# Kernel optimization log

Measured on AMD Instinct MI355X. Metric: run time of the kernel, lower is better.

The kernel has to match this reference:

```python
import jax, jax.numpy as jnp
import numpy as np
from functools import partial

D, H, W = 32, 256, 256   # grid_size (D, H, W)
V = 40000                # number of active voxels
C_IN, C_OUT = 16, 32
K = 3                    # kernel size
P = 32                   # max_points per voxel
EPS = 1e-5               # BatchNorm eps


def setup_inputs() -> dict:
    key = jax.random.key(0)
    k1, k2, k3, k4 = jax.random.split(key, 4)
    voxels = jax.random.normal(k1, (V, C_IN, P), dtype=jnp.float32)
    lin = jax.random.choice(k2, D * H * W, (V,), replace=False)
    d = (lin // (H * W)).astype(jnp.int32)
    h = ((lin // W) % H).astype(jnp.int32)
    w = (lin % W).astype(jnp.int32)
    indices = jnp.stack([w, h, d], axis=1)  # columns are (w, h, d) per original usage
    conv_w = jax.random.normal(k3, (C_OUT, C_IN, K, K, K), dtype=jnp.float32) * 0.05
    conv_b = jax.random.normal(k4, (C_OUT,), dtype=jnp.float32) * 0.05
    gamma = jnp.ones((C_OUT,), dtype=jnp.float32)
    beta = jnp.zeros((C_OUT,), dtype=jnp.float32)
    return {"voxels": voxels, "indices": indices, "conv_w": conv_w,
            "conv_b": conv_b, "gamma": gamma, "beta": beta, "batch_size": 1}


def reference(voxels, indices, conv_w, conv_b, gamma, beta, batch_size):
    # voxel features: mean over points  [V, C]
    feats = voxels.mean(axis=2)
    w_i, h_i, d_i = indices[:, 0], indices[:, 1], indices[:, 2]
    # original: batch_mask = indices[:,0] >= 0, plus per-dim bounds check
    valid = ((w_i >= 0) & (w_i < W) & (h_i >= 0) & (h_i < H) & (d_i >= 0) & (d_i < D))
    d_s = jnp.where(valid, d_i, D)  # route invalid rows out-of-bounds -> dropped
    # fused scatter replacing the python per-voxel loop; [D, H, W, C]
    grid = jnp.zeros((D, H, W, C_IN), dtype=voxels.dtype).at[d_s, h_i, w_i].set(
        feats, mode="drop")
    # same scatter is written into every batch slice in the original
    dense = jnp.broadcast_to(jnp.transpose(grid, (3, 0, 1, 2))[None],
                             (batch_size, C_IN, D, H, W))
    # Conv3d, padding = K//2 (SAME)
    out = jax.lax.conv_general_dilated(
        dense, conv_w, window_strides=(1, 1, 1), padding=[(K // 2, K // 2)] * 3,
        dimension_numbers=("NCDHW", "OIDHW", "NCDHW"))
    out = out + conv_b[None, :, None, None, None]
    # BatchNorm3d (training-mode batch statistics, biased variance)
    mean = out.mean(axis=(0, 2, 3, 4), keepdims=True)
    var = out.var(axis=(0, 2, 3, 4), keepdims=True)
    out = (out - mean) * jax.lax.rsqrt(var + EPS)
    out = out * gamma[None, :, None, None, None] + beta[None, :, None, None, None]
    return jax.nn.relu(out)
```

## Files before the change

### kernel.cpp

```cpp
#include <hip/hip_runtime.h>

#define D_   32
#define H_   256
#define W_   256
#define HW_  (H_ * W_)
#define DHW_ (D_ * H_ * W_)
#define V_   40000
#define CIN  16
#define COUT 32
#define P_   32
#define EPS_ 1e-5f

#define TD 2
#define TH 8
#define TW 32
#define NTX (W_ / TW)
#define NTY (H_ / TH)
#define NTZ (D_ / TD)
#define NT  (NTX * NTY * NTZ)
#define TPOS (TD * TH * TW)
#define OH 16
#define TAP_CAP 768

__global__ void bin_count_kernel(const int* __restrict__ idxs, int* __restrict__ counts) {
    int v = blockIdx.x * 256 + threadIdx.x;
    if (v >= V_) return;
    int w = idxs[3 * v], h = idxs[3 * v + 1], d = idxs[3 * v + 2];
    if ((unsigned)w < W_ && (unsigned)h < H_ && (unsigned)d < D_) {
        int b = (d / TD) * NTY * NTX + (h / TH) * NTX + (w / TW);
        atomicAdd(&counts[b], 1);
    }
}

__global__ void scan_kernel(const int* __restrict__ counts, int* __restrict__ starts,
                            int* __restrict__ cursor, const float* __restrict__ conv_w,
                            float4* __restrict__ wt4) {
    __shared__ int part[256];
    int t = threadIdx.x;
    int base = t * 16;
    int s = 0;
    for (int j = 0; j < 16; ++j) s += counts[base + j];
    part[t] = s;
    __syncthreads();
    for (int off = 1; off < 256; off <<= 1) {
        int val = part[t];
        int add = (t >= off) ? part[t - off] : 0;
        __syncthreads();
        part[t] = val + add;
        __syncthreads();
    }
    int run = (t > 0) ? part[t - 1] : 0;
    for (int j = 0; j < 16; ++j) {
        starts[base + j] = run;
        cursor[base + j] = run;
        run += counts[base + j];
    }
    for (int n = t; n < 2 * 27 * 4 * 16; n += 256) {
        int oo = n & 15;
        int jj = (n >> 4) & 3;
        int m  = n >> 6;
        int k  = m % 27;
        int half = m / 27;
        int o = half * 16 + oo;
        float4 wv;
        wv.x = conv_w[(o * CIN + 4 * jj + 0) * 27 + k];
        wv.y = conv_w[(o * CIN + 4 * jj + 1) * 27 + k];
        wv.z = conv_w[(o * CIN + 4 * jj + 2) * 27 + k];
        wv.w = conv_w[(o * CIN + 4 * jj + 3) * 27 + k];
        wt4[n] = wv;
    }
}

__global__ void bin_fill_kernel(const int* __restrict__ idxs, int* __restrict__ cursor,
                                int* __restrict__ pos_packed, int* __restrict__ perm) {
    int v = blockIdx.x * 256 + threadIdx.x;
    if (v >= V_) return;
    int w = idxs[3 * v], h = idxs[3 * v + 1], d = idxs[3 * v + 2];
    if ((unsigned)w < W_ && (unsigned)h < H_ && (unsigned)d < D_) {
        int b = (d / TD) * NTY * NTX + (h / TH) * NTX + (w / TW);
        int p = atomicAdd(&cursor[b], 1);
        pos_packed[p] = (d << 16) | (h << 8) | w;
        perm[v] = p;
    }
}

__global__ void featpack_kernel(const float* __restrict__ vox, const int* __restrict__ idxs,
                                const int* __restrict__ perm, float4* __restrict__ feats4) {
    int idx = blockIdx.x * 256 + threadIdx.x;
    if (idx >= V_ * 4) return;
    int v = idx >> 2, q = idx & 3;
    int w = idxs[3 * v], h = idxs[3 * v + 1], d = idxs[3 * v + 2];
    if (!((unsigned)w < W_ && (unsigned)h < H_ && (unsigned)d < D_)) return;
    int slot = perm[v];
    const float* base = vox + ((size_t)v * CIN + 4 * q) * P_;
    float m[4];
#pragma unroll
    for (int c = 0; c < 4; ++c) {
        const float4* p = (const float4*)(base + c * P_);
        float s = 0.f;
#pragma unroll
        for (int j = 0; j < P_ / 4; ++j) {
            float4 t = p[j];
            s += t.x + t.y + t.z + t.w;
        }
        m[c] = s * (1.0f / (float)P_);
    }
    feats4[slot * 4 + q] = make_float4(m[0], m[1], m[2], m[3]);
}

__global__ void __launch_bounds__(256, 2) tile_conv_kernel(
    const float4* __restrict__ feats4, const float4* __restrict__ wt4,
    const int* __restrict__ starts, const int* __restrict__ counts,
    const int* __restrict__ pos_packed, float* __restrict__ stats,
    float* __restrict__ out)
{
    __shared__ float  tile[TPOS * 16];
    __shared__ float4 wsm4[27 * 4 * 16];
    __shared__ int    taps[TAP_CAP];
    __shared__ int    seg_off[28];
    __shared__ int    seg_gs[27];
    __shared__ float  wsum[4][16], wsq[4][16];
    __shared__ int    ntap;

    int t = threadIdx.x;
    int tile_id = blockIdx.x;
    int half = blockIdx.y;
    int tx = tile_id % NTX, ty = (tile_id / NTX) % NTY, tz = tile_id / (NTX * NTY);
    int w0 = tx * TW, h0 = ty * TH, d0 = tz * TD;
    int obase = half * OH;

    for (int j = t; j < TPOS * 16 / 4; j += 256) ((float4*)tile)[j] = make_float4(0, 0, 0, 0);
    for (int j = t; j < 27 * 4 * 16; j += 256) wsm4[j] = wt4[half * (27 * 4 * 16) + j];
    if (t < 27) {
        int dz = t / 9 - 1, dy = (t / 3) % 3 - 1, dx = t % 3 - 1;
        int nz = tz + dz, ny = ty + dy, nx = tx + dx;
        int cnt = 0, gs = 0;
        if ((unsigned)nz < NTZ && (unsigned)ny < NTY && (unsigned)nx < NTX) {
            int b = nz * NTY * NTX + ny * NTX + nx;
            gs = starts[b];
            cnt = counts[b];
        }
        seg_gs[t] = gs;
        seg_off[t] = cnt;
    }
    if (t == 0) ntap = 0;
    __syncthreads();
    if (t == 0) {
        int run = 0;
#pragma unroll
        for (int i = 0; i < 27; ++i) {
            int c = seg_off[i];
            seg_off[i] = run;
            run += c;
        }
        seg_off[27] = run;
    }
    __syncthreads();
    int ncand = seg_off[27];

    for (int j = t; j < ncand; j += 256) {
        int b = 0;
        while (seg_off[b + 1] <= j) ++b;
        int src = seg_gs[b] + (j - seg_off[b]);
        int pp = pos_packed[src];
        int vw = pp & 255, vh = (pp >> 8) & 255, vd = pp >> 16;
        int dlo = max(vd - 1, d0), dhi = min(vd + 1, d0 + TD - 1);
        int hlo = max(vh - 1, h0), hhi = min(vh + 1, h0 + TH - 1);
        int wlo = max(vw - 1, w0), whi = min(vw + 1, w0 + TW - 1);
        for (int dq = dlo; dq <= dhi; ++dq)
            for (int hq = hlo; hq <= hhi; ++hq)
                for (int wq = wlo; wq <= whi; ++wq) {
                    int k = ((vd - dq + 1) * 3 + (vh - hq + 1)) * 3 + (vw - wq + 1);
                    int pos = ((dq - d0) * TH + (hq - h0)) * TW + (wq - w0);
                    int slot2 = atomicAdd(&ntap, 1);
                    if (slot2 < TAP_CAP) taps[slot2] = (src << 14) | (k << 9) | pos;
                }
    }
    __syncthreads();
    int nt = min(ntap, TAP_CAP);

    int oo = t & 15;
    int slot = t >> 4;
    for (int j = slot; j < nt; j += 16) {
        unsigned tap = (unsigned)taps[j];
        int pos = tap & 511;
        int k = (tap >> 9) & 31;
        int src = tap >> 14;
        const float4* fp = feats4 + src * 4;
        float4 f0 = fp[0], f1 = fp[1], f2 = fp[2], f3 = fp[3];
        const float4* wp = &wsm4[(k * 4) * 16 + oo];
        float4 q0 = wp[0], q1 = wp[16], q2 = wp[32], q3 = wp[48];
        float acc = q0.x * f0.x + q0.y * f0.y + q0.z * f0.z + q0.w * f0.w
                  + q1.x * f1.x + q1.y * f1.y + q1.z * f1.z + q1.w * f1.w
                  + q2.x * f2.x + q2.y * f2.y + q2.z * f2.z + q2.w * f2.w
                  + q3.x * f3.x + q3.y * f3.y + q3.z * f3.z + q3.w * f3.w;
        atomicAdd(&tile[pos * 16 + (oo ^ (pos & 15))], acc);
    }
    __syncthreads();

    float s1 = 0.f, s2 = 0.f;
    for (int p = slot; p < TPOS; p += 16) {
        float sv = tile[p * 16 + (oo ^ (p & 15))];
        s1 += sv;
        s2 += sv * sv;
    }
    s1 += __shfl_xor(s1, 16); s2 += __shfl_xor(s2, 16);
    s1 += __shfl_xor(s1, 32); s2 += __shfl_xor(s2, 32);
    int wave = t >> 6, lane = t & 63;
    if (lane < 16) { wsum[wave][lane] = s1; wsq[wave][lane] = s2; }

    int wl = t & 31;
    for (int r = t >> 5; r < OH * TD * TH; r += 8) {
        int oo2 = r >> 4;
        int rem = r & 15;
        int pos = rem * TW + wl;
        int dl = rem >> 3, hl = rem & 7;
        out[(size_t)(obase + oo2) * DHW_ + (size_t)(d0 + dl) * HW_ +
            (size_t)(h0 + hl) * W_ + (w0 + wl)] = tile[pos * 16 + (oo2 ^ (pos & 15))];
    }
    __syncthreads();
    if (t < 16) {
        float a = wsum[0][t] + wsum[1][t] + wsum[2][t] + wsum[3][t];
        float b = wsq[0][t] + wsq[1][t] + wsq[2][t] + wsq[3][t];
        atomicAdd(&stats[obase + t], a);
        atomicAdd(&stats[COUT + obase + t], b);
    }
}

__global__ void finalize_kernel(const float* __restrict__ stats,
                                const float* __restrict__ gamma,
                                const float* __restrict__ beta,
                                float* __restrict__ mi) {
    int t = threadIdx.x;
    if (t < COUT) {
        float n = (float)DHW_;
        float m1 = stats[t] / n;
        float m2 = stats[COUT + t] / n;
        float var = fmaxf(m2 - m1 * m1, 0.f);
        float inv = rsqrtf(var + EPS_);
        float A = gamma[t] * inv;
        mi[t] = A;
        mi[COUT + t] = -m1 * A + beta[t];
    }
}

__global__ void norm_kernel(float* __restrict__ out, const float* __restrict__ mi) {
    int idx4 = blockIdx.x * 256 + threadIdx.x;
    int c = idx4 >> 19;
    float A = mi[c], B = mi[COUT + c];
    float4 x = ((const float4*)out)[idx4];
    x.x = fmaxf(x.x * A + B, 0.f);
    x.y = fmaxf(x.y * A + B, 0.f);
    x.z = fmaxf(x.z * A + B, 0.f);
    x.w = fmaxf(x.w * A + B, 0.f);
    ((float4*)out)[idx4] = x;
}

extern "C" void kernel_launch(void* const* d_in, const int* in_sizes, int n_in,
                              void* d_out, int out_size, void* d_ws, size_t ws_size,
                              hipStream_t stream) {
    const float* voxels  = (const float*)d_in[0];
    const int*   indices = (const int*)  d_in[1];
    const float* conv_w  = (const float*)d_in[2];
    const float* gamma   = (const float*)d_in[4];
    const float* beta    = (const float*)d_in[5];
    float* out = (float*)d_out;

    float4* wt4     = (float4*)d_ws;
    float4* feats4  = wt4 + 3456;
    int*    counts  = (int*)(feats4 + (size_t)V_ * 4);
    int*    starts  = counts + NT;
    int*    cursor  = starts + NT;
    int*    pos_pk  = cursor + NT;
    int*    perm    = pos_pk + V_;
    float*  stats   = (float*)(perm + V_);
    float*  mi      = stats + 2 * COUT;

    hipMemsetAsync(counts, 0, NT * sizeof(int), stream);
    hipMemsetAsync(stats, 0, 2 * COUT * sizeof(float), stream);

    bin_count_kernel<<<(V_ + 255) / 256, 256, 0, stream>>>(indices, counts);
    scan_kernel<<<1, 256, 0, stream>>>(counts, starts, cursor, conv_w, wt4);
    bin_fill_kernel<<<(V_ + 255) / 256, 256, 0, stream>>>(indices, cursor, pos_pk, perm);
    featpack_kernel<<<(V_ * 4 + 255) / 256, 256, 0, stream>>>(voxels, indices, perm, feats4);

    dim3 grid(NT, 2);
    tile_conv_kernel<<<grid, 256, 0, stream>>>(feats4, wt4, starts, counts, pos_pk,
                                               stats, out);
    finalize_kernel<<<1, 64, 0, stream>>>(stats, gamma, beta, mi);

    const int n4 = COUT * DHW_ / 4;
    norm_kernel<<<n4 / 256, 256, 0, stream>>>(out, mi);
}
```

Baseline: 752.2 us.

## Precompute global tap lists and recompute conv to fuse BN+ReLU into output write

Replaces per-tile candidate gathering with a global scatter of taps into per-tile lists, built from a count/scan/fill pass over voxels. The conv kernel now runs twice: the first pass only gathers BN statistics without writing output, and the second recomputes the sparse conv and writes the normalized, ReLU'd result directly. This removes the separate norm kernel's full read-modify-write over the large dense output. Feature means are now computed in voxel order, so the permutation step goes away. The cost is recomputing the sparse conv and a larger global tap buffer, and blocks move to 512 threads.

```diff
diff --git a/kernel.cpp b/kernel.cpp
--- a/kernel.cpp
+++ b/kernel.cpp
@@ -20,15 +20,37 @@
 #define NT  (NTX * NTY * NTZ)
 #define TPOS (TD * TH * TW)
 #define OH 16
-#define TAP_CAP 768
-
-__global__ void bin_count_kernel(const int* __restrict__ idxs, int* __restrict__ counts) {
+
+__global__ void feats_kernel(const float* __restrict__ vox, float* __restrict__ feats) {
+    int idx = blockIdx.x * 256 + threadIdx.x;
+    if (idx >= V_ * CIN) return;
+    const float4* p = (const float4*)(vox + (size_t)idx * P_);
+    float s = 0.f;
+#pragma unroll
+    for (int j = 0; j < P_ / 4; ++j) {
+        float4 q = p[j];
+        s += q.x + q.y + q.z + q.w;
+    }
+    feats[idx] = s * (1.0f / (float)P_);
+}
+
+__global__ void tap_count_kernel(const int* __restrict__ idxs, int* __restrict__ counts) {
     int v = blockIdx.x * 256 + threadIdx.x;
     if (v >= V_) return;
     int w = idxs[3 * v], h = idxs[3 * v + 1], d = idxs[3 * v + 2];
-    if ((unsigned)w < W_ && (unsigned)h < H_ && (unsigned)d < D_) {
-        int b = (d / TD) * NTY * NTX + (h / TH) * NTX + (w / TW);
-        atomicAdd(&counts[b], 1);
+    if (!((unsigned)w < W_ && (unsigned)h < H_ && (unsigned)d < D_)) return;
+    int dlo = max(d - 1, 0), dhi = min(d + 1, D_ - 1);
+    int hlo = max(h - 1, 0), hhi = min(h + 1, H_ - 1);
+    int wlo = max(w - 1, 0), whi = min(w + 1, W_ - 1);
+    for (int tz = dlo / TD; tz <= dhi / TD; ++tz) {
+        int nd = min(dhi, tz * TD + TD - 1) - max(dlo, tz * TD) + 1;
+        for (int ty = hlo / TH; ty <= hhi / TH; ++ty) {
+            int nh = min(hhi, ty * TH + TH - 1) - max(hlo, ty * TH) + 1;
+            for (int tx = wlo / TW; tx <= whi / TW; ++tx) {
+                int nw = min(whi, tx * TW + TW - 1) - max(wlo, tx * TW) + 1;
+                atomicAdd(&counts[(tz * NTY + ty) * NTX + tx], nd * nh * nw);
+            }
+        }
     }
 }
 
@@ -71,56 +93,46 @@
     }
 }
 
-__global__ void bin_fill_kernel(const int* __restrict__ idxs, int* __restrict__ cursor,
-                                int* __restrict__ pos_packed, int* __restrict__ perm) {
+__global__ void tap_fill_kernel(const int* __restrict__ idxs, int* __restrict__ cursor,
+                                int* __restrict__ taps_g) {
     int v = blockIdx.x * 256 + threadIdx.x;
     if (v >= V_) return;
     int w = idxs[3 * v], h = idxs[3 * v + 1], d = idxs[3 * v + 2];
-    if ((unsigned)w < W_ && (unsigned)h < H_ && (unsigned)d < D_) {
-        int b = (d / TD) * NTY * NTX + (h / TH) * NTX + (w / TW);
-        int p = atomicAdd(&cursor[b], 1);
-        pos_packed[p] = (d << 16) | (h << 8) | w;
-        perm[v] = p;
-    }
-}
-
-__global__ void featpack_kernel(const float* __restrict__ vox, const int* __restrict__ idxs,
-                                const int* __restrict__ perm, float4* __restrict__ feats4) {
-    int idx = blockIdx.x * 256 + threadIdx.x;
-    if (idx >= V_ * 4) return;
-    int v = idx >> 2, q = idx & 3;
-    int w = idxs[3 * v], h = idxs[3 * v + 1], d = idxs[3 * v + 2];
     if (!((unsigned)w < W_ && (unsigned)h < H_ && (unsigned)d < D_)) return;
-    int slot = perm[v];
-    const float* base = vox + ((size_t)v * CIN + 4 * q) * P_;
-    float m[4];
-#pragma unroll
-    for (int c = 0; c < 4; ++c) {
-        const float4* p = (const float4*)(base + c * P_);
-        float s = 0.f;
-#pragma unroll
-        for (int j = 0; j < P_ / 4; ++j) {
-            float4 t = p[j];
-            s += t.x + t.y + t.z + t.w;
-        }
-        m[c] = s * (1.0f / (float)P_);
-    }
-    feats4[slot * 4 + q] = make_float4(m[0], m[1], m[2], m[3]);
-}
-
-__global__ void __launch_bounds__(256, 2) tile_conv_kernel(
+    int dlo = max(d - 1, 0), dhi = min(d + 1, D_ - 1);
+    int hlo = max(h - 1, 0), hhi = min(h + 1, H_ - 1);
+    int wlo = max(w - 1, 0), whi = min(w + 1, W_ - 1);
+    for (int tz = dlo / TD; tz <= dhi / TD; ++tz) {
+        int sdlo = max(dlo, tz * TD), sdhi = min(dhi, tz * TD + TD - 1);
+        for (int ty = hlo / TH; ty <= hhi / TH; ++ty) {
+            int shlo = max(hlo, ty * TH), shhi = min(hhi, ty * TH + TH - 1);
+            for (int tx = wlo / TW; tx <= whi / TW; ++tx) {
+                int swlo = max(wlo, tx * TW), swhi = min(whi, tx * TW + TW - 1);
+                int cnt = (sdhi - sdlo + 1) * (shhi - shlo + 1) * (swhi - swlo + 1);
+                int p = atomicAdd(&cursor[(tz * NTY + ty) * NTX + tx], cnt);
+                for (int dq = sdlo; dq <= sdhi; ++dq)
+                    for (int hq = shlo; hq <= shhi; ++hq)
+                        for (int wq = swlo; wq <= swhi; ++wq) {
+                            int k = ((d - dq + 1) * 3 + (h - hq + 1)) * 3 + (w - wq + 1);
+                            int pos = ((dq - tz * TD) * TH + (hq - ty * TH)) * TW +
+                                      (wq - tx * TW);
+                            taps_g[p++] = (v << 14) | (k << 9) | pos;
+                        }
+            }
+        }
+    }
+}
+
+template <int PASS>
+__global__ void __launch_bounds__(512, 4) tile_conv_kernel(
     const float4* __restrict__ feats4, const float4* __restrict__ wt4,
     const int* __restrict__ starts, const int* __restrict__ counts,
-    const int* __restrict__ pos_packed, float* __restrict__ stats,
-    float* __restrict__ out)
+    const int* __restrict__ taps_g, float* __restrict__ stats,
+    const float* __restrict__ mi, float* __restrict__ out)
 {
     __shared__ float  tile[TPOS * 16];
     __shared__ float4 wsm4[27 * 4 * 16];
-    __shared__ int    taps[TAP_CAP];
-    __shared__ int    seg_off[28];
-    __shared__ int    seg_gs[27];
-    __shared__ float  wsum[4][16], wsq[4][16];
-    __shared__ int    ntap;
+    __shared__ float  wsum[8][16], wsq[8][16];
 
     int t = threadIdx.x;
     int tile_id = blockIdx.x;
@@ -129,60 +141,17 @@
     int w0 = tx * TW, h0 = ty * TH, d0 = tz * TD;
     int obase = half * OH;
 
-    for (int j = t; j < TPOS * 16 / 4; j += 256) ((float4*)tile)[j] = make_float4(0, 0, 0, 0);
-    for (int j = t; j < 27 * 4 * 16; j += 256) wsm4[j] = wt4[half * (27 * 4 * 16) + j];
-    if (t < 27) {
-        int dz = t / 9 - 1, dy = (t / 3) % 3 - 1, dx = t % 3 - 1;
-        int nz = tz + dz, ny = ty + dy, nx = tx + dx;
-        int cnt = 0, gs = 0;
-        if ((unsigned)nz < NTZ && (unsigned)ny < NTY && (unsigned)nx < NTX) {
-            int b = nz * NTY * NTX + ny * NTX + nx;
-            gs = starts[b];
-            cnt = counts[b];
-        }
-        seg_gs[t] = gs;
-        seg_off[t] = cnt;
-    }
-    if (t == 0) ntap = 0;
+    for (int j = t; j < TPOS * 16 / 4; j += 512) ((float4*)tile)[j] = make_float4(0, 0, 0, 0);
+    for (int j = t; j < 27 * 4 * 16; j += 512) wsm4[j] = wt4[half * (27 * 4 * 16) + j];
     __syncthreads();
-    if (t == 0) {
-        int run = 0;
-#pragma unroll
-        for (int i = 0; i < 27; ++i) {
-            int c = seg_off[i];
-            seg_off[i] = run;
-            run += c;
-        }
-        seg_off[27] = run;
-    }
-    __syncthreads();
-    int ncand = seg_off[27];
-
-    for (int j = t; j < ncand; j += 256) {
-        int b = 0;
-        while (seg_off[b + 1] <= j) ++b;
-        int src = seg_gs[b] + (j - seg_off[b]);
-        int pp = pos_packed[src];
-        int vw = pp & 255, vh = (pp >> 8) & 255, vd = pp >> 16;
-        int dlo = max(vd - 1, d0), dhi = min(vd + 1, d0 + TD - 1);
-        int hlo = max(vh - 1, h0), hhi = min(vh + 1, h0 + TH - 1);
-        int wlo = max(vw - 1, w0), whi = min(vw + 1, w0 + TW - 1);
-        for (int dq = dlo; dq <= dhi; ++dq)
-            for (int hq = hlo; hq <= hhi; ++hq)
-                for (int wq = wlo; wq <= whi; ++wq) {
-                    int k = ((vd - dq + 1) * 3 + (vh - hq + 1)) * 3 + (vw - wq + 1);
-                    int pos = ((dq - d0) * TH + (hq - h0)) * TW + (wq - w0);
-                    int slot2 = atomicAdd(&ntap, 1);
-                    if (slot2 < TAP_CAP) taps[slot2] = (src << 14) | (k << 9) | pos;
-                }
-    }
-    __syncthreads();
-    int nt = min(ntap, TAP_CAP);
-
-    int oo = t & 15;
+
+    int base = starts[tile_id];
+    int cnt  = counts[tile_id];
+    int oo   = t & 15;
     int slot = t >> 4;
-    for (int j = slot; j < nt; j += 16) {
-        unsigned tap = (unsigned)taps[j];
+
+    for (int j = slot; j < cnt; j += 32) {
+        unsigned tap = (unsigned)taps_g[base + j];
         int pos = tap & 511;
         int k = (tap >> 9) & 31;
         int src = tap >> 14;
@@ -198,32 +167,38 @@
     }
     __syncthreads();
 
-    float s1 = 0.f, s2 = 0.f;
-    for (int p = slot; p < TPOS; p += 16) {
-        float sv = tile[p * 16 + (oo ^ (p & 15))];
-        s1 += sv;
-        s2 += sv * sv;
-    }
-    s1 += __shfl_xor(s1, 16); s2 += __shfl_xor(s2, 16);
-    s1 += __shfl_xor(s1, 32); s2 += __shfl_xor(s2, 32);
-    int wave = t >> 6, lane = t & 63;
-    if (lane < 16) { wsum[wave][lane] = s1; wsq[wave][lane] = s2; }
-
-    int wl = t & 31;
-    for (int r = t >> 5; r < OH * TD * TH; r += 8) {
-        int oo2 = r >> 4;
-        int rem = r & 15;
-        int pos = rem * TW + wl;
-        int dl = rem >> 3, hl = rem & 7;
-        out[(size_t)(obase + oo2) * DHW_ + (size_t)(d0 + dl) * HW_ +
-            (size_t)(h0 + hl) * W_ + (w0 + wl)] = tile[pos * 16 + (oo2 ^ (pos & 15))];
-    }
-    __syncthreads();
-    if (t < 16) {
-        float a = wsum[0][t] + wsum[1][t] + wsum[2][t] + wsum[3][t];
-        float b = wsq[0][t] + wsq[1][t] + wsq[2][t] + wsq[3][t];
-        atomicAdd(&stats[obase + t], a);
-        atomicAdd(&stats[COUT + obase + t], b);
+    if (PASS == 1) {
+        float s1 = 0.f, s2 = 0.f;
+        for (int p = slot; p < TPOS; p += 32) {
+            float sv = tile[p * 16 + (oo ^ (p & 15))];
+            s1 += sv;
+            s2 += sv * sv;
+        }
+        s1 += __shfl_xor(s1, 16); s2 += __shfl_xor(s2, 16);
+        s1 += __shfl_xor(s1, 32); s2 += __shfl_xor(s2, 32);
+        int wave = t >> 6, lane = t & 63;
+        if (lane < 16) { wsum[wave][lane] = s1; wsq[wave][lane] = s2; }
+        __syncthreads();
+        if (t < 16) {
+            float a = 0.f, b = 0.f;
+#pragma unroll
+            for (int wv = 0; wv < 8; ++wv) { a += wsum[wv][t]; b += wsq[wv][t]; }
+            atomicAdd(&stats[obase + t], a);
+            atomicAdd(&stats[COUT + obase + t], b);
+        }
+    } else {
+        int wl = t & 31;
+        for (int r = t >> 5; r < OH * TD * TH; r += 16) {
+            int oo2 = r >> 4;
+            int rem = r & 15;
+            int o = obase + oo2;
+            float A = mi[o], B = mi[COUT + o];
+            int pos = rem * TW + wl;
+            float s = tile[pos * 16 + (oo2 ^ (pos & 15))];
+            int dl = rem >> 3, hl = rem & 7;
+            out[(size_t)o * DHW_ + (size_t)(d0 + dl) * HW_ + (size_t)(h0 + hl) * W_ +
+                (w0 + wl)] = fmaxf(s * A + B, 0.f);
+        }
     }
 }
 
@@ -244,18 +219,6 @@
     }
 }
 
-__global__ void norm_kernel(float* __restrict__ out, const float* __restrict__ mi) {
-    int idx4 = blockIdx.x * 256 + threadIdx.x;
-    int c = idx4 >> 19;
-    float A = mi[c], B = mi[COUT + c];
-    float4 x = ((const float4*)out)[idx4];
-    x.x = fmaxf(x.x * A + B, 0.f);
-    x.y = fmaxf(x.y * A + B, 0.f);
-    x.z = fmaxf(x.z * A + B, 0.f);
-    x.w = fmaxf(x.w * A + B, 0.f);
-    ((float4*)out)[idx4] = x;
-}
-
 extern "C" void kernel_launch(void* const* d_in, const int* in_sizes, int n_in,
                               void* d_out, int out_size, void* d_ws, size_t ws_size,
                               hipStream_t stream) {
@@ -266,29 +229,27 @@
     const float* beta    = (const float*)d_in[5];
     float* out = (float*)d_out;
 
-    float4* wt4     = (float4*)d_ws;
-    float4* feats4  = wt4 + 3456;
-    int*    counts  = (int*)(feats4 + (size_t)V_ * 4);
-    int*    starts  = counts + NT;
-    int*    cursor  = starts + NT;
-    int*    pos_pk  = cursor + NT;
-    int*    perm    = pos_pk + V_;
-    float*  stats   = (float*)(perm + V_);
-    float*  mi      = stats + 2 * COUT;
+    float4* wt4    = (float4*)d_ws;
+    float*  feats  = (float*)(wt4 + 3456);
+    int*    counts = (int*)(feats + (size_t)V_ * CIN);
+    int*    starts = counts + NT;
+    int*    cursor = starts + NT;
+    int*    taps_g = cursor + NT;
+    float*  stats  = (float*)(taps_g + (size_t)V_ * 27);
+    float*  mi     = stats + 2 * COUT;
 
     hipMemsetAsync(counts, 0, NT * sizeof(int), stream);
     hipMemsetAsync(stats, 0, 2 * COUT * sizeof(float), stream);
 
-    bin_count_kernel<<<(V_ + 255) / 256, 256, 0, stream>>>(indices, counts);
+    feats_kernel<<<(V_ * CIN + 255) / 256, 256, 0, stream>>>(voxels, feats);
+    tap_count_kernel<<<(V_ + 255) / 256, 256, 0, stream>>>(indices, counts);
     scan_kernel<<<1, 256, 0, stream>>>(counts, starts, cursor, conv_w, wt4);
-    bin_fill_kernel<<<(V_ + 255) / 256, 256, 0, stream>>>(indices, cursor, pos_pk, perm);
-    featpack_kernel<<<(V_ * 4 + 255) / 256, 256, 0, stream>>>(voxels, indices, perm, feats4);
+    tap_fill_kernel<<<(V_ + 255) / 256, 256, 0, stream>>>(indices, cursor, taps_g);
 
     dim3 grid(NT, 2);
-    tile_conv_kernel<<<grid, 256, 0, stream>>>(feats4, wt4, starts, counts, pos_pk,
-                                               stats, out);
+    tile_conv_kernel<1><<<grid, 512, 0, stream>>>((const float4*)feats, wt4, starts,
+                                                  counts, taps_g, stats, mi, out);
     finalize_kernel<<<1, 64, 0, stream>>>(stats, gamma, beta, mi);
-
-    const int n4 = COUT * DHW_ / 4;
-    norm_kernel<<<n4 / 256, 256, 0, stream>>>(out, mi);
-}
+    tile_conv_kernel<2><<<grid, 512, 0, stream>>>((const float4*)feats, wt4, starts,
+                                                  counts, taps_g, stats, mi, out);
+}
```

New measurement: 825.5 us. 9.7% more time.
